# Optimization experiments

Measured on AMD Instinct MI355X. Metric: run time of the kernel, lower is better.

## Reference

```python
import jax, jax.numpy as jnp
import numpy as np

NUM_HEADS = 8
LN_EPS = 1e-5


def setup_inputs() -> dict:
    key = jax.random.key(0)
    ks = jax.random.split(key, 12)
    N, H, G = 100000, 512, 256
    s = 1.0 / np.sqrt(H)
    return {
        "x": jax.random.normal(ks[0], (N, H), dtype=jnp.float32),
        "batch": jnp.sort(jax.random.randint(ks[1], (N,), 0, G)),
        "query": jax.random.normal(ks[2], (H,), dtype=jnp.float32),
        "k_w": jax.random.uniform(ks[3], (H, H), minval=-s, maxval=s, dtype=jnp.float32),
        "k_b": jax.random.uniform(ks[4], (H,), minval=-s, maxval=s, dtype=jnp.float32),
        "v_w": jax.random.uniform(ks[5], (H, H), minval=-s, maxval=s, dtype=jnp.float32),
        "v_b": jax.random.uniform(ks[6], (H,), minval=-s, maxval=s, dtype=jnp.float32),
        "o_w": jax.random.uniform(ks[7], (H, H), minval=-s, maxval=s, dtype=jnp.float32),
        "o_b": jax.random.uniform(ks[8], (H,), minval=-s, maxval=s, dtype=jnp.float32),
        "ln_g": jnp.ones((H,), dtype=jnp.float32),
        "ln_b": jnp.zeros((H,), dtype=jnp.float32),
        "num_graphs": 256,
    }


def reference(x, batch, query, k_w, k_b, v_w, v_b, o_w, o_b, ln_g, ln_b, num_graphs):
    N, H = x.shape
    nh = NUM_HEADS
    hd = H // nh
    # projections (torch Linear: x @ W.T + b)
    k = (x @ k_w.T + k_b).reshape(N, nh, hd)
    v = (x @ v_w.T + v_b).reshape(N, nh, hd)
    q = query.reshape(nh, hd)
    # per-node, per-head attention logits against the shared graph query
    s = jnp.einsum("nhd,hd->nh", k, q) / np.float32(np.sqrt(hd))  # [N, nh]
    # segment softmax over nodes of each graph (stable via segment max)
    s_max = jax.ops.segment_max(s, batch, num_segments=num_graphs)  # [G, nh]
    w = jnp.exp(s - s_max[batch])  # [N, nh]
    denom = jax.ops.segment_sum(w, batch, num_segments=num_graphs)  # [G, nh]
    numer = jax.ops.segment_sum(w[:, :, None] * v, batch, num_segments=num_graphs)  # [G, nh, hd]
    attended = numer / jnp.where(denom > 0, denom, 1.0)[:, :, None]  # zeros for empty graphs
    out = attended.reshape(num_graphs, H)
    out = out @ o_w.T + o_b
    # layer norm over last dim
    mu = out.mean(-1, keepdims=True)
    var = out.var(-1, keepdims=True)
    out = (out - mu) / jnp.sqrt(var + LN_EPS) * ln_g + ln_b
    return out
```

## Files before the change

kernel.cpp:

```cpp
#include <hip/hip_runtime.h>
#include <math.h>

#define H 512
#define NH 8
#define NG 256

#define WS_QK   0
#define WS_SB   4096
#define WS_SEG  4352
#define WS_VWT  8192
#define WS_OWT  270336


__global__ __launch_bounds__(256) void k_setup(
    const int* __restrict__ batch, int N, int* __restrict__ seg,
    const float* __restrict__ k_w, const float* __restrict__ k_b,
    const float* __restrict__ query, float* __restrict__ qk, float* __restrict__ sb,
    const float* __restrict__ vw, const float* __restrict__ ow,
    float* __restrict__ vwt, float* __restrict__ owt) {
  __shared__ float tile[32][33];
  const int b = blockIdx.x;
  if (b < 2) {
    int g = b * 256 + threadIdx.x;
    if (g > NG) return;
    int lo = 0, hi = N;
    while (lo < hi) { int mid = (lo + hi) >> 1; if (batch[mid] < g) lo = mid + 1; else hi = mid; }
    seg[g] = lo;
  } else if (b < 18) {
    int gt = (b - 2) * 256 + threadIdx.x;
    int h = gt >> 9, j = gt & 511;
    float a = 0.f;
#pragma unroll 8
    for (int d = 0; d < 64; ++d)
      a = fmaf(k_w[(size_t)(h * 64 + d) * H + j], query[h * 64 + d], a);
    qk[j * 8 + h] = a * 0.125f;
    if (gt < 8) {
      float s = 0.f;
      for (int d = 0; d < 64; ++d) s = fmaf(k_b[gt * 64 + d], query[gt * 64 + d], s);
      sb[gt] = s * 0.125f;
    }
  } else {
    int bb = b - 18;
    const float* in  = (bb < 256) ? vw  : ow;
    float*       out = (bb < 256) ? vwt : owt;
    int tidx = bb & 255;
    int bx = tidx & 15, by = tidx >> 4;
    int tx = threadIdx.x & 31, ty = threadIdx.x >> 5;
#pragma unroll
    for (int k = 0; k < 4; ++k)
      tile[ty + 8 * k][tx] = in[(size_t)(by * 32 + ty + 8 * k) * H + bx * 32 + tx];
    __syncthreads();
#pragma unroll
    for (int k = 0; k < 4; ++k)
      out[(size_t)(bx * 32 + ty + 8 * k) * H + by * 32 + tx] = tile[tx][ty + 8 * k];
  }
}


#define DPP_ADD(v, ctrl, rmask)                                                   \
  v += __int_as_float(__builtin_amdgcn_update_dpp(0, __float_as_int(v), ctrl,     \
                                                  rmask, 0xf, true))

__global__ __launch_bounds__(512, 2) void k_graph(
    const float* __restrict__ x, const float* __restrict__ qk, const float* __restrict__ sb,
    const int* __restrict__ seg, const float* __restrict__ vwt, const float* __restrict__ vb,
    const float* __restrict__ owt, const float* __restrict__ ob,
    const float* __restrict__ lng, const float* __restrict__ lnb,
    float* __restrict__ out) {
  const int g = blockIdx.x;
  const int t = threadIdx.x;
  const int lane = t & 63, wid = t >> 6;
  const int s0 = seg[g], e0 = seg[g + 1];

  __shared__ float TA[8][512];
  __shared__ float TB[8][512];
  __shared__ float den_lds[8][8];
  __shared__ float att[512];
  __shared__ float den_s[8], dinv_s[8];
  __shared__ float redA[8], redB[8];

  float qk_r[8][8];
#pragma unroll
  for (int ci = 0; ci < 8; ++ci) {
    int j = (ci < 4) ? (4 * lane + ci) : (256 + 4 * lane + ci - 4);
    const float4* row = (const float4*)(qk + j * 8);
    float4 q0 = row[0], q1 = row[1];
    qk_r[ci][0] = q0.x; qk_r[ci][1] = q0.y; qk_r[ci][2] = q0.z; qk_r[ci][3] = q0.w;
    qk_r[ci][4] = q1.x; qk_r[ci][5] = q1.y; qk_r[ci][6] = q1.z; qk_r[ci][7] = q1.w;
  }
  float sbr[8];
#pragma unroll
  for (int h = 0; h < 8; ++h) sbr[h] = sb[h];

  float T_r[8][8];
  float den[8];
#pragma unroll
  for (int h = 0; h < 8; ++h) {
    den[h] = 0.f;
#pragma unroll
    for (int ci = 0; ci < 8; ++ci) T_r[h][ci] = 0.f;
  }

  const float4* x4 = (const float4*)x;
  int n = s0 + wid;
  float4 b0a, b0b, b1a, b1b;
  if (n < e0)     { size_t a = (size_t)n * 128 + lane;       b0a = x4[a]; b0b = x4[a + 64]; }
  if (n + 8 < e0) { size_t a = (size_t)(n + 8) * 128 + lane; b1a = x4[a]; b1b = x4[a + 64]; }

  for (; n < e0; n += 8) {
    float4 b2a, b2b;
    if (n + 16 < e0) { size_t a = (size_t)(n + 16) * 128 + lane; b2a = x4[a]; b2b = x4[a + 64]; }

    float xv[8] = {b0a.x, b0a.y, b0a.z, b0a.w, b0b.x, b0b.y, b0b.z, b0b.w};
    float pp[8] = {0.f, 0.f, 0.f, 0.f, 0.f, 0.f, 0.f, 0.f};
#pragma unroll
    for (int ci = 0; ci < 8; ++ci)
#pragma unroll
      for (int h = 0; h < 8; ++h) pp[h] = fmaf(xv[ci], qk_r[ci][h], pp[h]);

#pragma unroll
    for (int h = 0; h < 8; ++h) DPP_ADD(pp[h], 0x111, 0xf);
#pragma unroll
    for (int h = 0; h < 8; ++h) DPP_ADD(pp[h], 0x112, 0xf);
#pragma unroll
    for (int h = 0; h < 8; ++h) DPP_ADD(pp[h], 0x114, 0xf);
#pragma unroll
    for (int h = 0; h < 8; ++h) DPP_ADD(pp[h], 0x118, 0xf);
#pragma unroll
    for (int h = 0; h < 8; ++h) DPP_ADD(pp[h], 0x142, 0xa);
#pragma unroll
    for (int h = 0; h < 8; ++h) DPP_ADD(pp[h], 0x143, 0xc);

    float w[8];
#pragma unroll
    for (int h = 0; h < 8; ++h) {
      float s = __int_as_float(__builtin_amdgcn_readlane(__float_as_int(pp[h]), 63));
      w[h] = __expf(s + sbr[h]);
      den[h] += w[h];
    }
#pragma unroll
    for (int h = 0; h < 8; ++h)
#pragma unroll
      for (int ci = 0; ci < 8; ++ci) T_r[h][ci] = fmaf(w[h], xv[ci], T_r[h][ci]);

    b0a = b1a; b0b = b1b; b1a = b2a; b1b = b2b;
  }

  if (lane == 0) {
#pragma unroll
    for (int h = 0; h < 8; ++h) den_lds[wid][h] = den[h];
  }
  for (int s = 0; s < 4; ++s) {
    if (wid == s || wid == s + 4) {
      float (*T_)[512] = (wid < 4) ? TA : TB;
#pragma unroll
      for (int h = 0; h < 8; ++h) {
        float4 v0 = make_float4(T_r[h][0], T_r[h][1], T_r[h][2], T_r[h][3]);
        float4 v1 = make_float4(T_r[h][4], T_r[h][5], T_r[h][6], T_r[h][7]);
        float4* d0 = (float4*)&T_[h][4 * lane];
        float4* d1 = (float4*)&T_[h][256 + 4 * lane];
        if (s == 0) { *d0 = v0; *d1 = v1; }
        else {
          float4 o0 = *d0, o1 = *d1;
          o0.x += v0.x; o0.y += v0.y; o0.z += v0.z; o0.w += v0.w;
          o1.x += v1.x; o1.y += v1.y; o1.z += v1.z; o1.w += v1.w;
          *d0 = o0; *d1 = o1;
        }
      }
    }
    __syncthreads();
  }
#pragma unroll
  for (int h = 0; h < 8; ++h) TA[h][t] += TB[h][t];
  if (t < 8) {
    float d = 0.f;
#pragma unroll
    for (int w = 0; w < 8; ++w) d += den_lds[w][t];
    den_s[t] = d;
    dinv_s[t] = (d > 0.f) ? 1.f / d : 1.f;
  }
  __syncthreads();

  const int h = t >> 6;
  const float* Th = TA[h];
  float a = 0.f;
#pragma unroll 16
  for (int j = 0; j < H; ++j)
    a = fmaf(Th[j], vwt[(size_t)j * H + t], a);
  att[t] = (a + den_s[h] * vb[t]) * dinv_s[h];
  __syncthreads();

  float o = ob[t];
#pragma unroll 16
  for (int k = 0; k < H; ++k)
    o = fmaf(att[k], owt[(size_t)k * H + t], o);

  float r1 = o, r2 = o * o;
#pragma unroll
  for (int m = 1; m < 64; m <<= 1) { r1 += __shfl_xor(r1, m, 64); r2 += __shfl_xor(r2, m, 64); }
  if (lane == 0) { redA[wid] = r1; redB[wid] = r2; }
  __syncthreads();
  float S1 = 0.f, S2 = 0.f;
#pragma unroll
  for (int w = 0; w < 8; ++w) { S1 += redA[w]; S2 += redB[w]; }
  float mu = S1 * (1.f / 512.f);
  float var = S2 * (1.f / 512.f) - mu * mu;
  float rs = rsqrtf(var + 1e-5f);
  out[(size_t)g * H + t] = (o - mu) * rs * lng[t] + lnb[t];
}


extern "C" void kernel_launch(void* const* d_in, const int* in_sizes, int n_in,
                              void* d_out, int out_size, void* d_ws, size_t ws_size,
                              hipStream_t stream) {
  const float* x     = (const float*)d_in[0];
  const int*   batch = (const int*)d_in[1];
  const float* query = (const float*)d_in[2];
  const float* k_w   = (const float*)d_in[3];
  const float* k_b   = (const float*)d_in[4];
  const float* v_w   = (const float*)d_in[5];
  const float* v_b   = (const float*)d_in[6];
  const float* o_w   = (const float*)d_in[7];
  const float* o_b   = (const float*)d_in[8];
  const float* ln_g  = (const float*)d_in[9];
  const float* ln_b  = (const float*)d_in[10];
  const int N = in_sizes[0] / H;

  float* ws  = (float*)d_ws;
  float* qk  = ws + WS_QK;
  float* sb  = ws + WS_SB;
  int*   seg = (int*)(ws + WS_SEG);
  float* vwt = ws + WS_VWT;
  float* owt = ws + WS_OWT;

  hipLaunchKernelGGL(k_setup, dim3(530), dim3(256), 0, stream,
                     batch, N, seg, k_w, k_b, query, qk, sb, v_w, o_w, vwt, owt);
  hipLaunchKernelGGL(k_graph, dim3(NG), dim3(512), 0, stream,
                     x, qk, sb, seg, vwt, v_b, owt, o_b, ln_g, ln_b, (float*)d_out);
}
```

Before: 341.7 us.

## Store transposed V/O weights as packed bf16 and stream x with nontemporal loads

The setup kernel now transposes v_w and o_w into bf16 pairs packed in 32-bit words, which halves the weight bytes each graph block reads in its two 512x512 matvecs. The graph kernel unpacks each word into two floats and accumulates in fp32. Loads of x are switched to nontemporal loads so the one-pass streaming read of x does not pollute the cache. Rounding the weights to bf16 adds error compared with the fp32 reference.

```diff
diff --git a/kernel.cpp b/kernel.cpp
--- a/kernel.cpp
+++ b/kernel.cpp
@@ -4,12 +4,19 @@
 #define H 512
 #define NH 8
 #define NG 256
+
+typedef float f32x4 __attribute__((ext_vector_type(4)));
 
 #define WS_QK   0
 #define WS_SB   4096
 #define WS_SEG  4352
 #define WS_VWT  8192
-#define WS_OWT  270336
+#define WS_OWT  139264
+
+static __device__ __forceinline__ unsigned int bf16r(float f) {
+  unsigned int u = __float_as_uint(f);
+  return (u + 0x7FFFu + ((u >> 16) & 1u)) >> 16;
+}
 
 
 __global__ __launch_bounds__(256) void k_setup(
@@ -17,7 +24,7 @@
     const float* __restrict__ k_w, const float* __restrict__ k_b,
     const float* __restrict__ query, float* __restrict__ qk, float* __restrict__ sb,
     const float* __restrict__ vw, const float* __restrict__ ow,
-    float* __restrict__ vwt, float* __restrict__ owt) {
+    unsigned int* __restrict__ vwt, unsigned int* __restrict__ owt) {
   __shared__ float tile[32][33];
   const int b = blockIdx.x;
   if (b < 2) {
@@ -41,8 +48,8 @@
     }
   } else {
     int bb = b - 18;
-    const float* in  = (bb < 256) ? vw  : ow;
-    float*       out = (bb < 256) ? vwt : owt;
+    const float*  in   = (bb < 256) ? vw  : ow;
+    unsigned int* outw = (bb < 256) ? vwt : owt;
     int tidx = bb & 255;
     int bx = tidx & 15, by = tidx >> 4;
     int tx = threadIdx.x & 31, ty = threadIdx.x >> 5;
@@ -51,8 +58,12 @@
       tile[ty + 8 * k][tx] = in[(size_t)(by * 32 + ty + 8 * k) * H + bx * 32 + tx];
     __syncthreads();
 #pragma unroll
-    for (int k = 0; k < 4; ++k)
-      out[(size_t)(bx * 32 + ty + 8 * k) * H + by * 32 + tx] = tile[tx][ty + 8 * k];
+    for (int k = 0; k < 2; ++k) {
+      int wr = ty + 8 * k;
+      unsigned int lo = bf16r(tile[tx][2 * wr]);
+      unsigned int hi = bf16r(tile[tx][2 * wr + 1]);
+      outw[(size_t)(bx * 16 + wr) * H + by * 32 + tx] = (hi << 16) | lo;
+    }
   }
 }
 
@@ -63,10 +74,10 @@
 
 __global__ __launch_bounds__(512, 2) void k_graph(
     const float* __restrict__ x, const float* __restrict__ qk, const float* __restrict__ sb,
-    const int* __restrict__ seg, const float* __restrict__ vwt, const float* __restrict__ vb,
-    const float* __restrict__ owt, const float* __restrict__ ob,
-    const float* __restrict__ lng, const float* __restrict__ lnb,
-    float* __restrict__ out) {
+    const int* __restrict__ seg, const unsigned int* __restrict__ vwt,
+    const float* __restrict__ vb, const unsigned int* __restrict__ owt,
+    const float* __restrict__ ob, const float* __restrict__ lng,
+    const float* __restrict__ lnb, float* __restrict__ out) {
   const int g = blockIdx.x;
   const int t = threadIdx.x;
   const int lane = t & 63, wid = t >> 6;
@@ -101,15 +112,21 @@
     for (int ci = 0; ci < 8; ++ci) T_r[h][ci] = 0.f;
   }
 
-  const float4* x4 = (const float4*)x;
+  const f32x4* x4 = (const f32x4*)x;
   int n = s0 + wid;
-  float4 b0a, b0b, b1a, b1b;
-  if (n < e0)     { size_t a = (size_t)n * 128 + lane;       b0a = x4[a]; b0b = x4[a + 64]; }
-  if (n + 8 < e0) { size_t a = (size_t)(n + 8) * 128 + lane; b1a = x4[a]; b1b = x4[a + 64]; }
+  f32x4 b0a, b0b, b1a, b1b;
+  if (n < e0)     { size_t a = (size_t)n * 128 + lane;
+                    b0a = __builtin_nontemporal_load(&x4[a]);
+                    b0b = __builtin_nontemporal_load(&x4[a + 64]); }
+  if (n + 8 < e0) { size_t a = (size_t)(n + 8) * 128 + lane;
+                    b1a = __builtin_nontemporal_load(&x4[a]);
+                    b1b = __builtin_nontemporal_load(&x4[a + 64]); }
 
   for (; n < e0; n += 8) {
-    float4 b2a, b2b;
-    if (n + 16 < e0) { size_t a = (size_t)(n + 16) * 128 + lane; b2a = x4[a]; b2b = x4[a + 64]; }
+    f32x4 b2a, b2b;
+    if (n + 16 < e0) { size_t a = (size_t)(n + 16) * 128 + lane;
+                       b2a = __builtin_nontemporal_load(&x4[a]);
+                       b2b = __builtin_nontemporal_load(&x4[a + 64]); }
 
     float xv[8] = {b0a.x, b0a.y, b0a.z, b0a.w, b0b.x, b0b.y, b0b.z, b0b.w};
     float pp[8] = {0.f, 0.f, 0.f, 0.f, 0.f, 0.f, 0.f, 0.f};
@@ -184,16 +201,26 @@
   const int h = t >> 6;
   const float* Th = TA[h];
   float a = 0.f;
-#pragma unroll 16
-  for (int j = 0; j < H; ++j)
-    a = fmaf(Th[j], vwt[(size_t)j * H + t], a);
+#pragma unroll 8
+  for (int jw = 0; jw < H / 2; ++jw) {
+    unsigned int u = vwt[(size_t)jw * H + t];
+    float w0 = __uint_as_float(u << 16);
+    float w1 = __uint_as_float(u & 0xFFFF0000u);
+    a = fmaf(Th[2 * jw], w0, a);
+    a = fmaf(Th[2 * jw + 1], w1, a);
+  }
   att[t] = (a + den_s[h] * vb[t]) * dinv_s[h];
   __syncthreads();
 
   float o = ob[t];
-#pragma unroll 16
-  for (int k = 0; k < H; ++k)
-    o = fmaf(att[k], owt[(size_t)k * H + t], o);
+#pragma unroll 8
+  for (int kw = 0; kw < H / 2; ++kw) {
+    unsigned int u = owt[(size_t)kw * H + t];
+    float w0 = __uint_as_float(u << 16);
+    float w1 = __uint_as_float(u & 0xFFFF0000u);
+    o = fmaf(att[2 * kw], w0, o);
+    o = fmaf(att[2 * kw + 1], w1, o);
+  }
 
   float r1 = o, r2 = o * o;
 #pragma unroll
@@ -230,8 +257,8 @@
   float* qk  = ws + WS_QK;
   float* sb  = ws + WS_SB;
   int*   seg = (int*)(ws + WS_SEG);
-  float* vwt = ws + WS_VWT;
-  float* owt = ws + WS_OWT;
+  unsigned int* vwt = (unsigned int*)(ws + WS_VWT);
+  unsigned int* owt = (unsigned int*)(ws + WS_OWT);
 
   hipLaunchKernelGGL(k_setup, dim3(530), dim3(256), 0, stream,
                      batch, N, seg, k_w, k_b, query, qk, sb, v_w, o_w, vwt, owt);
```

Measured after the change: 339.9 us. No clear change (-0.5%).
